# Optimization experiments

Measured on AMD Instinct MI355X. Metric: run time of the kernel, lower is better.

The kernel has to match this reference:

```python
import jax, jax.numpy as jnp
import numpy as np

N_NODES = 163842
N_EDGES = 983040
NUM_FEATURES = 22
LAYER_SIZES = [22, 32, 64, 64]
K = 3  # kernel_size
D = 2  # pseudo-coordinate dim
EPS = 1e-15


def _glorot(key, shape):
    fan = shape[0] + shape[-1]
    s = jnp.sqrt(6.0 / fan)
    return jax.random.uniform(key, shape, jnp.float32, -s, s)


def setup_inputs() -> dict:
    key = jax.random.key(0)
    ks = iter(jax.random.split(key, 64))
    inp = {
        'x': jax.random.normal(next(ks), (N_NODES, NUM_FEATURES), jnp.float32),
        'edge_index': jax.random.randint(next(ks), (2, N_EDGES), 0, N_NODES, jnp.int64),
        'edge_attr': jax.random.uniform(next(ks), (N_EDGES, D), jnp.float32),
    }
    for i, (cin, cout) in enumerate(zip(LAYER_SIZES[:-1], LAYER_SIZES[1:])):
        inp[f'g{i}'] = _glorot(next(ks), (cin, K * cout))
        inp[f'mu{i}'] = _glorot(next(ks), (K, D))
        inp[f'sigma{i}'] = jax.random.uniform(next(ks), (K, D), jnp.float32, 0.5, 1.5)
        inp[f'root{i}'] = _glorot(next(ks), (cin, cout))
        inp[f'b{i}'] = jnp.zeros((cout,), jnp.float32)
    inp['fc_w'] = _glorot(next(ks), (LAYER_SIZES[-1], 2))
    inp['fc_b'] = jnp.zeros((2,), jnp.float32)
    return inp


def gmm_conv(x, src, dst, pseudo, g, mu, sigma, root, bias):
    # PyG GMMConv, separate_gaussians=False, aggr='mean', root_weight=True
    n = x.shape[0]
    cout = root.shape[1]
    xw = (x @ g).reshape(n, K, cout)                       # [N, K, Cout]
    diff = pseudo[:, None, :] - mu[None, :, :]             # [E, K, D]
    gauss = jnp.exp(-0.5 * jnp.sum(diff * diff / (EPS + sigma[None] ** 2), axis=-1))  # [E, K]
    msg = jnp.einsum('ek,eko->eo', gauss, xw[src])         # [E, Cout]
    agg = jax.ops.segment_sum(msg, dst, num_segments=n)
    deg = jax.ops.segment_sum(jnp.ones((src.shape[0],), x.dtype), dst, num_segments=n)
    agg = agg / jnp.clip(deg, 1.0)[:, None]                # mean aggregation
    return agg + x @ root + bias


def reference(x, edge_index, edge_attr, g0, mu0, sigma0, root0, b0,
              g1, mu1, sigma1, root1, b1, g2, mu2, sigma2, root2, b2,
              fc_w, fc_b):
    src, dst = edge_index[0], edge_index[1]
    params = [(g0, mu0, sigma0, root0, b0),
              (g1, mu1, sigma1, root1, b1),
              (g2, mu2, sigma2, root2, b2)]
    h = x
    for (g, mu, sigma, root, b) in params:
        h = jax.nn.relu(gmm_conv(h, src, dst, edge_attr, g, mu, sigma, root, b))
    logits = h @ fc_w + fc_b                               # [N, 2]
    return jax.nn.log_softmax(logits, axis=1)
```

## Files before the change

kernel.cpp:

```cpp
#include <hip/hip_runtime.h>

#define NN 163842
#define NE 983040
#define NB 641
#define BC 32

using short8   = __attribute__((ext_vector_type(8))) short;
using ushort8v = __attribute__((ext_vector_type(8))) unsigned short;
using f32x4    = __attribute__((ext_vector_type(4))) float;

__global__ __launch_bounds__(256) void scatter_bucket(const int* __restrict__ dst,
                                                      int* __restrict__ cnt,
                                                      int* __restrict__ eidx, int E) {
    int e0 = blockIdx.x * 512 + threadIdx.x;
    int e1 = e0 + 256;
    int d0 = (e0 < E) ? dst[e0] : 0;
    int d1 = (e1 < E) ? dst[e1] : 0;
    int p0 = 0, p1 = 0;
    if (e0 < E) p0 = atomicAdd(&cnt[d0], 1);
    if (e1 < E) p1 = atomicAdd(&cnt[d1], 1);
    if (e0 < E && p0 < BC) eidx[d0 * BC + p0] = e0;
    if (e1 < E && p1 < BC) eidx[d1 * BC + p1] = e1;
}

__global__ __launch_bounds__(256) void scan1(const int* __restrict__ degi,
                                             int* __restrict__ cursor,
                                             int* __restrict__ bsum, int n) {
    __shared__ int tmp[256];
    int t = threadIdx.x;
    int i = blockIdx.x * 256 + t;
    int v = (i < n) ? min(degi[i], BC) : 0;
    tmp[t] = v;
    __syncthreads();
    for (int o = 1; o < 256; o <<= 1) {
        int x = (t >= o) ? tmp[t - o] : 0;
        __syncthreads();
        tmp[t] += x;
        __syncthreads();
    }
    if (i < n) cursor[i] = tmp[t] - v;
    if (t == 255) bsum[blockIdx.x] = tmp[255];
}

__global__ void scan2(int* __restrict__ bsum, int nb) {
    __shared__ int tmp[1024];
    int t = threadIdx.x;
    int v = (t < nb) ? bsum[t] : 0;
    tmp[t] = v;
    __syncthreads();
    for (int o = 1; o < 1024; o <<= 1) {
        int x = (t >= o) ? tmp[t - o] : 0;
        __syncthreads();
        tmp[t] += x;
        __syncthreads();
    }
    if (t < nb) bsum[t] = tmp[t] - v;
}

__global__ __launch_bounds__(256) void scan3(int* __restrict__ cursor,
                                             const int* __restrict__ bsum, int n) {
    int i = blockIdx.x * 256 + threadIdx.x;
    if (i < n) cursor[i] += bsum[blockIdx.x];
}

static __device__ __forceinline__ unsigned short bf16rne(float x) {
    unsigned u = __float_as_uint(x);
    u += 0x7FFFu + ((u >> 16) & 1u);
    return (unsigned short)(u >> 16);
}

static __device__ __forceinline__ float bf2f(unsigned short u) {
    return __uint_as_float(((unsigned)u) << 16);
}

template <int CIN, int CINP, int COUTR>
static __device__ __forceinline__ void wcb_emit(int t, const float* __restrict__ g,
                                                const float* __restrict__ root,
                                                unsigned short* __restrict__ Wcb) {
    constexpr int KTl = 4 * CINP;
    int nIdx = t / KTl, k = t - nIdx * KTl;
    int seg = k / CINP, c = k - seg * CINP;
    float v = 0.0f;
    if (c < CIN)
        v = (seg < 3) ? g[c * (3 * COUTR) + seg * COUTR + nIdx] : root[c * COUTR + nIdx];
    Wcb[t] = bf16rne(v);
}

__global__ __launch_bounds__(256) void gather_build(const int* __restrict__ eidx,
                                                    const int* __restrict__ cnt,
                                                    const int* __restrict__ cursor,
                                                    const int* __restrict__ src,
                                                    const float* __restrict__ ea,
                                                    float4* __restrict__ gedr,
                                                    const float* __restrict__ x,
                                                    unsigned short* __restrict__ xp,
                                                    const float* __restrict__ g0, const float* __restrict__ rt0,
                                                    const float* __restrict__ g1, const float* __restrict__ rt1,
                                                    const float* __restrict__ g2, const float* __restrict__ rt2,
                                                    unsigned short* __restrict__ W0,
                                                    unsigned short* __restrict__ W1,
                                                    unsigned short* __restrict__ W2,
                                                    int CBLK, int PBLK, int n) {
    int bid = blockIdx.x;
    if (bid < CBLK) {
        int node = bid * 32 + (threadIdx.x >> 3);
        int li   = threadIdx.x & 7;
        if (node >= n) return;
        int dgc = min(cnt[node], BC);
        int st  = cursor[node];
        for (int c = li; c < dgc; c += 8) {
            int e = eidx[node * BC + c];
            float2 exy = *(const float2*)(ea + 2 * (size_t)e);
            gedr[st + c] = make_float4(__int_as_float(src[e]), exy.x, exy.y, 0.0f);
        }
        return;
    }
    bid -= CBLK;
    if (bid < PBLK) {
        int r = bid * 256 + threadIdx.x;
        if (r >= n) return;
        float v[22];
        const float2* x2 = (const float2*)(x + (size_t)r * 22);
#pragma unroll
        for (int j = 0; j < 11; ++j) *(float2*)(v + 2 * j) = x2[j];
        unsigned short* op = xp + (size_t)r * 32;
#pragma unroll
        for (int g8 = 0; g8 < 4; ++g8) {
            ushort8v o;
#pragma unroll
            for (int j = 0; j < 8; ++j) {
                int c = g8 * 8 + j;
                o[j] = (c < 22) ? bf16rne(v[c]) : (unsigned short)0;
            }
            *(ushort8v*)(op + g8 * 8) = o;
        }
        return;
    }
    bid -= PBLK;
    int t = bid * 256 + threadIdx.x;
    constexpr int T0 = 32 * 128, T1 = 64 * 128, T2 = 64 * 256;
    if (t < T0)                wcb_emit<22, 32, 32>(t, g0, rt0, W0);
    else if (t < T0 + T1)      wcb_emit<32, 32, 64>(t - T0, g1, rt1, W1);
    else if (t < T0 + T1 + T2) wcb_emit<64, 64, 64>(t - T0 - T1, g2, rt2, W2);
}

static __device__ __forceinline__ void fma4(float4& a, float g, const float4& hv) {
    a.x = fmaf(g, hv.x, a.x);
    a.y = fmaf(g, hv.y, a.y);
    a.z = fmaf(g, hv.z, a.z);
    a.w = fmaf(g, hv.w, a.w);
}

static __device__ __forceinline__ float3 gauss3c(float ex, float ey,
                                                 const float* muv, const float* ccv) {
    float3 r;
    float dx, dy;
    dx = ex - muv[0]; dy = ey - muv[1];
    r.x = __expf(fmaf(ccv[0] * dx, dx, ccv[1] * dy * dy));
    dx = ex - muv[2]; dy = ey - muv[3];
    r.y = __expf(fmaf(ccv[2] * dx, dx, ccv[3] * dy * dy));
    dx = ex - muv[4]; dy = ey - muv[5];
    r.z = __expf(fmaf(ccv[4] * dx, dx, ccv[5] * dy * dy));
    return r;
}

template <int CINP, int COUTR, int NT, bool FC>
__global__ __launch_bounds__(NT, 8) void fused_mfma(const unsigned short* __restrict__ h, int hs,
                                                    const float4* __restrict__ ged,
                                                    const int* __restrict__ cursor,
                                                    const int* __restrict__ degi,
                                                    const unsigned short* __restrict__ Wcb,
                                                    const float* __restrict__ bias,
                                                    const float* __restrict__ mu,
                                                    const float* __restrict__ sg,
                                                    unsigned short* __restrict__ out,
                                                    const float* __restrict__ fcw,
                                                    const float* __restrict__ fcb,
                                                    float* __restrict__ fout, int n) {
    constexpr int KT    = 4 * CINP;
    constexpr int ST4   = KT / 8 + 1;
    constexpr int ROWU  = ST4 * 8;
    constexpr int NSTEP = KT / 32;
    constexpr int NCT   = COUTR / 16;
    constexpr int LPN   = CINP / 8;
    constexpr int NPP   = NT / LPN;
    static_assert(NPP == 64, "single pass over the 64-node tile");
    __shared__ float4 sa[64 * ST4];
    unsigned short* st = (unsigned short*)sa;
    const int row0 = blockIdx.x * 64;

    {
        float muv[6], ccv[6];
#pragma unroll
        for (int j = 0; j < 6; ++j) muv[j] = mu[j];
#pragma unroll
        for (int j = 0; j < 6; ++j) {
            float s = sg[j];
            ccv[j] = -0.5f / (1e-15f + s * s);
        }
        const int sub = threadIdx.x / LPN;
        const int li  = threadIdx.x % LPN;
        int node = row0 + sub; if (node > n - 1) node = n - 1;
        int p   = cursor[node];
        int dg  = min(degi[node], BC);
        int end = p + dg;
        float4 a[3][2];
#pragma unroll
        for (int k = 0; k < 3; ++k)
#pragma unroll
            for (int q = 0; q < 2; ++q) a[k][q] = make_float4(0, 0, 0, 0);
        for (; p < end; p += 2) {
            int q1 = (p + 1 < end) ? (p + 1) : p;
            float4 ed0 = ged[p];
            float4 ed1 = ged[q1];
            ushort8v hu0 = *(const ushort8v*)(h + (long)__float_as_int(ed0.x) * hs + li * 8);
            ushort8v hu1 = *(const ushort8v*)(h + (long)__float_as_int(ed1.x) * hs + li * 8);
            float3 g0 = gauss3c(ed0.y, ed0.z, muv, ccv);
            float3 g1 = gauss3c(ed1.y, ed1.z, muv, ccv);
            if (p + 1 >= end) { g1.x = 0.0f; g1.y = 0.0f; g1.z = 0.0f; }
            {
                float4 h0 = make_float4(bf2f(hu0[0]), bf2f(hu0[1]), bf2f(hu0[2]), bf2f(hu0[3]));
                float4 h1 = make_float4(bf2f(hu0[4]), bf2f(hu0[5]), bf2f(hu0[6]), bf2f(hu0[7]));
                fma4(a[0][0], g0.x, h0); fma4(a[0][1], g0.x, h1);
                fma4(a[1][0], g0.y, h0); fma4(a[1][1], g0.y, h1);
                fma4(a[2][0], g0.z, h0); fma4(a[2][1], g0.z, h1);
            }
            {
                float4 h0 = make_float4(bf2f(hu1[0]), bf2f(hu1[1]), bf2f(hu1[2]), bf2f(hu1[3]));
                float4 h1 = make_float4(bf2f(hu1[4]), bf2f(hu1[5]), bf2f(hu1[6]), bf2f(hu1[7]));
                fma4(a[0][0], g1.x, h0); fma4(a[0][1], g1.x, h1);
                fma4(a[1][0], g1.y, h0); fma4(a[1][1], g1.y, h1);
                fma4(a[2][0], g1.z, h0); fma4(a[2][1], g1.z, h1);
            }
        }
        float inv = 1.0f / (float)max(dg, 1);
#pragma unroll
        for (int k = 0; k < 3; ++k)
#pragma unroll
            for (int q = 0; q < 2; ++q) fma4(a[k][q], inv - 1.0f, a[k][q]);
        ushort8v hv8 = *(const ushort8v*)(h + (long)node * hs + li * 8);
        int base = sub * ROWU;
        int c8b  = li * 8;
#pragma unroll
        for (int k = 0; k < 3; ++k) {
            ushort8v v;
            v[0] = bf16rne(a[k][0].x); v[1] = bf16rne(a[k][0].y);
            v[2] = bf16rne(a[k][0].z); v[3] = bf16rne(a[k][0].w);
            v[4] = bf16rne(a[k][1].x); v[5] = bf16rne(a[k][1].y);
            v[6] = bf16rne(a[k][1].z); v[7] = bf16rne(a[k][1].w);
            *(ushort8v*)(st + base + k * CINP + c8b) = v;
        }
        *(ushort8v*)(st + base + 3 * CINP + c8b) = hv8;
    }
    __syncthreads();

    constexpr int NW    = NT / 64;
    constexpr int TILES = 4 * NCT;
    constexpr int TPW   = TILES / NW;
    constexpr int RST   = NW / NCT;
    static_assert(NW % NCT == 0 && TILES % NW == 0, "tile remap");
    const int lane = threadIdx.x & 63;
    const int wv   = threadIdx.x >> 6;
    const int quad = lane >> 4;
    const int c16  = lane & 15;
    const int ct   = wv % NCT;
    const int rg0  = wv / NCT;
    f32x4 acc[TPW];
#pragma unroll
    for (int i = 0; i < TPW; ++i) acc[i] = (f32x4){0.0f, 0.0f, 0.0f, 0.0f};
    const unsigned short* bcol = Wcb + (ct * 16 + c16) * KT;
#pragma unroll
    for (int s = 0; s < NSTEP; ++s) {
        short8 bf = *(const short8*)(bcol + s * 32 + quad * 8);
#pragma unroll
        for (int i = 0; i < TPW; ++i) {
            const unsigned short* arow = st + (16 * (rg0 + i * RST) + c16) * ROWU;
            short8 af = *(const short8*)(arow + s * 32 + quad * 8);
            acc[i] = __builtin_amdgcn_mfma_f32_16x16x32_bf16(af, bf, acc[i], 0, 0, 0);
        }
    }
    if constexpr (!FC) {
#pragma unroll
        for (int i = 0; i < TPW; ++i) {
            int rg  = rg0 + i * RST;
            int col = ct * 16 + c16;
            float b = bias[col];
#pragma unroll
            for (int r = 0; r < 4; ++r) {
                int grow = row0 + rg * 16 + quad * 4 + r;
                if (grow < n)
                    out[(long)grow * COUTR + col] = bf16rne(fmaxf(acc[i][r] + b, 0.0f));
            }
        }
    } else {
        static_assert(COUTR == 64, "FC fusion assumes 64-wide rows");
        constexpr int FS = 72;
        __syncthreads();
        {
            int col = ct * 16 + c16;
            float b = bias[col];
#pragma unroll
            for (int i = 0; i < TPW; ++i) {
                int rg = rg0 + i * RST;
#pragma unroll
                for (int r = 0; r < 4; ++r) {
                    int lr2 = rg * 16 + quad * 4 + r;
                    st[lr2 * FS + col] = bf16rne(fmaxf(acc[i][r] + b, 0.0f));
                }
            }
        }
        __syncthreads();
        int t = threadIdx.x;
        if (t < 64) {
            int node = row0 + t;
            if (node < n) {
                const ushort8v* hr = (const ushort8v*)(st + t * FS);
                float l0 = fcb[0];
                float l1 = fcb[1];
#pragma unroll
                for (int j8 = 0; j8 < 8; ++j8) {
                    ushort8v hv = hr[j8];
#pragma unroll
                    for (int j = 0; j < 8; ++j) {
                        float hvf = bf2f(hv[j]);
                        l0 = fmaf(hvf, fcw[2 * (8 * j8 + j)], l0);
                        l1 = fmaf(hvf, fcw[2 * (8 * j8 + j) + 1], l1);
                    }
                }
                float mx  = fmaxf(l0, l1);
                float lse = mx + logf(__expf(l0 - mx) + __expf(l1 - mx));
                fout[2 * (long)node]     = l0 - lse;
                fout[2 * (long)node + 1] = l1 - lse;
            }
        }
    }
}

extern "C" void kernel_launch(void* const* d_in, const int* in_sizes, int n_in,
                              void* d_out, int out_size, void* d_ws, size_t ws_size,
                              hipStream_t stream) {
    const float* x   = (const float*)d_in[0];
    const int*   ei  = (const int*)d_in[1];
    const float* ea  = (const float*)d_in[2];
    const float* g_[3]  = {(const float*)d_in[3],  (const float*)d_in[8],  (const float*)d_in[13]};
    const float* mu_[3] = {(const float*)d_in[4],  (const float*)d_in[9],  (const float*)d_in[14]};
    const float* sg_[3] = {(const float*)d_in[5],  (const float*)d_in[10], (const float*)d_in[15]};
    const float* rt_[3] = {(const float*)d_in[6],  (const float*)d_in[11], (const float*)d_in[16]};
    const float* bs_[3] = {(const float*)d_in[7],  (const float*)d_in[12], (const float*)d_in[17]};
    const float* fcw = (const float*)d_in[18];
    const float* fcb = (const float*)d_in[19];
    float* out = (float*)d_out;
    (void)in_sizes; (void)n_in; (void)out_size; (void)ws_size;

    char* w = (char*)d_ws;
    size_t off = 0;
    auto carve = [&](size_t bytes) -> void* {
        void* p = (void*)(w + off);
        off += (bytes + 255) & ~(size_t)255;
        return p;
    };
    int*    cnt    = (int*)carve((size_t)NN * 4);
    int*    cursor = (int*)carve((size_t)NN * 4);
    int*    eidx   = (int*)carve((size_t)NN * BC * 4);
    float4* gedr   = (float4*)carve((size_t)NE * 16);
    int*    bsum   = (int*)carve(1024 * 4);
    unsigned short* W0 = (unsigned short*)carve((size_t)32 * 128 * 2);
    unsigned short* W1 = (unsigned short*)carve((size_t)64 * 128 * 2);
    unsigned short* W2 = (unsigned short*)carve((size_t)64 * 256 * 2);
    unsigned short* xp = (unsigned short*)carve((size_t)NN * 32 * 2);
    unsigned short* hA = (unsigned short*)carve((size_t)NN * 32 * 2);
    unsigned short* hB = (unsigned short*)carve((size_t)NN * 64 * 2);

    const int* src = ei;
    const int* dst = ei + NE;
    const int CB = (NN + 31) / 32;
    const int PB = (NN + 255) / 256;
    const int WB = 112;
    const int GB = (NN + 63) / 64;

    hipMemsetAsync(cnt, 0, (size_t)NN * 4, stream);
    scatter_bucket<<<(NE + 511) / 512, 256, 0, stream>>>(dst, cnt, eidx, NE);
    scan1<<<NB, 256, 0, stream>>>(cnt, cursor, bsum, NN);
    scan2<<<1, 1024, 0, stream>>>(bsum, NB);
    scan3<<<NB, 256, 0, stream>>>(cursor, bsum, NN);
    gather_build<<<CB + PB + WB, 256, 0, stream>>>(eidx, cnt, cursor, src, ea, gedr, x, xp,
                                                   g_[0], rt_[0], g_[1], rt_[1], g_[2], rt_[2],
                                                   W0, W1, W2, CB, PB, NN);

    fused_mfma<32, 32, 256, false><<<GB, 256, 0, stream>>>(xp, 32, gedr, cursor, cnt,
                                                           W0, bs_[0], mu_[0], sg_[0],
                                                           hA, nullptr, nullptr,
                                                           nullptr, NN);
    fused_mfma<32, 64, 256, false><<<GB, 256, 0, stream>>>(hA, 32, gedr, cursor, cnt,
                                                           W1, bs_[1], mu_[1], sg_[1],
                                                           hB, nullptr, nullptr,
                                                           nullptr, NN);
    fused_mfma<64, 64, 512, true><<<GB, 512, 0, stream>>>(hB, 64, gedr, cursor, cnt,
                                                          W2, bs_[2], mu_[2], sg_[2],
                                                          nullptr, fcw, fcb,
                                                          out, NN);
}
```

Before: 322.4 us.

## Precompute per-layer Gaussian edge weights in gather pass and use packed float math

The gather pass now evaluates the three Gaussian kernel weights for every edge and every layer once, storing a separate src+weights float4 stream per layer. The fused layer kernels no longer compute exp per edge per lane group. The aggregation loop switches to packed v2f bf16 unpacking and multiply-adds. The workspace is reorganised so the edge bucket array aliases the hidden-state buffers, which avoids a larger allocation. The cost is two extra edge streams written per run, about 32 MB of added write traffic in the preprocessing kernel.

```diff
diff --git a/kernel.cpp b/kernel.cpp
--- a/kernel.cpp
+++ b/kernel.cpp
@@ -8,6 +8,7 @@
 using short8   = __attribute__((ext_vector_type(8))) short;
 using ushort8v = __attribute__((ext_vector_type(8))) unsigned short;
 using f32x4    = __attribute__((ext_vector_type(4))) float;
+using v2f      = __attribute__((ext_vector_type(2))) float;
 
 __global__ __launch_bounds__(256) void scatter_bucket(const int* __restrict__ dst,
                                                       int* __restrict__ cnt,
@@ -69,8 +70,11 @@
     return (unsigned short)(u >> 16);
 }
 
-static __device__ __forceinline__ float bf2f(unsigned short u) {
-    return __uint_as_float(((unsigned)u) << 16);
+static __device__ __forceinline__ v2f bfpair(unsigned u) {
+    v2f r;
+    r[0] = __uint_as_float(u << 16);
+    r[1] = __uint_as_float(u & 0xffff0000u);
+    return r;
 }
 
 template <int CIN, int CINP, int COUTR>
@@ -86,12 +90,30 @@
     Wcb[t] = bf16rne(v);
 }
 
+static __device__ __forceinline__ float3 gauss3c(float ex, float ey,
+                                                 const float* muv, const float* ccv) {
+    float3 r;
+    float dx, dy;
+    dx = ex - muv[0]; dy = ey - muv[1];
+    r.x = __expf(fmaf(ccv[0] * dx, dx, ccv[1] * dy * dy));
+    dx = ex - muv[2]; dy = ey - muv[3];
+    r.y = __expf(fmaf(ccv[2] * dx, dx, ccv[3] * dy * dy));
+    dx = ex - muv[4]; dy = ey - muv[5];
+    r.z = __expf(fmaf(ccv[4] * dx, dx, ccv[5] * dy * dy));
+    return r;
+}
+
 __global__ __launch_bounds__(256) void gather_build(const int* __restrict__ eidx,
                                                     const int* __restrict__ cnt,
                                                     const int* __restrict__ cursor,
                                                     const int* __restrict__ src,
                                                     const float* __restrict__ ea,
-                                                    float4* __restrict__ gedr,
+                                                    const float* __restrict__ mu0, const float* __restrict__ sg0,
+                                                    const float* __restrict__ mu1, const float* __restrict__ sg1,
+                                                    const float* __restrict__ mu2, const float* __restrict__ sg2,
+                                                    float4* __restrict__ ged0,
+                                                    float4* __restrict__ ged1,
+                                                    float4* __restrict__ ged2,
                                                     const float* __restrict__ x,
                                                     unsigned short* __restrict__ xp,
                                                     const float* __restrict__ g0, const float* __restrict__ rt0,
@@ -103,6 +125,15 @@
                                                     int CBLK, int PBLK, int n) {
     int bid = blockIdx.x;
     if (bid < CBLK) {
+        float muv0[6], ccv0[6], muv1[6], ccv1[6], muv2[6], ccv2[6];
+#pragma unroll
+        for (int j = 0; j < 6; ++j) {
+            muv0[j] = mu0[j]; muv1[j] = mu1[j]; muv2[j] = mu2[j];
+            float s0 = sg0[j], s1 = sg1[j], s2 = sg2[j];
+            ccv0[j] = -0.5f / (1e-15f + s0 * s0);
+            ccv1[j] = -0.5f / (1e-15f + s1 * s1);
+            ccv2[j] = -0.5f / (1e-15f + s2 * s2);
+        }
         int node = bid * 32 + (threadIdx.x >> 3);
         int li   = threadIdx.x & 7;
         if (node >= n) return;
@@ -111,7 +142,13 @@
         for (int c = li; c < dgc; c += 8) {
             int e = eidx[node * BC + c];
             float2 exy = *(const float2*)(ea + 2 * (size_t)e);
-            gedr[st + c] = make_float4(__int_as_float(src[e]), exy.x, exy.y, 0.0f);
+            float sb = __int_as_float(src[e]);
+            float3 G0 = gauss3c(exy.x, exy.y, muv0, ccv0);
+            float3 G1 = gauss3c(exy.x, exy.y, muv1, ccv1);
+            float3 G2 = gauss3c(exy.x, exy.y, muv2, ccv2);
+            ged0[st + c] = make_float4(sb, G0.x, G0.y, G0.z);
+            ged1[st + c] = make_float4(sb, G1.x, G1.y, G1.z);
+            ged2[st + c] = make_float4(sb, G2.x, G2.y, G2.z);
         }
         return;
     }
@@ -142,26 +179,6 @@
     if (t < T0)                wcb_emit<22, 32, 32>(t, g0, rt0, W0);
     else if (t < T0 + T1)      wcb_emit<32, 32, 64>(t - T0, g1, rt1, W1);
     else if (t < T0 + T1 + T2) wcb_emit<64, 64, 64>(t - T0 - T1, g2, rt2, W2);
-}
-
-static __device__ __forceinline__ void fma4(float4& a, float g, const float4& hv) {
-    a.x = fmaf(g, hv.x, a.x);
-    a.y = fmaf(g, hv.y, a.y);
-    a.z = fmaf(g, hv.z, a.z);
-    a.w = fmaf(g, hv.w, a.w);
-}
-
-static __device__ __forceinline__ float3 gauss3c(float ex, float ey,
-                                                 const float* muv, const float* ccv) {
-    float3 r;
-    float dx, dy;
-    dx = ex - muv[0]; dy = ey - muv[1];
-    r.x = __expf(fmaf(ccv[0] * dx, dx, ccv[1] * dy * dy));
-    dx = ex - muv[2]; dy = ey - muv[3];
-    r.y = __expf(fmaf(ccv[2] * dx, dx, ccv[3] * dy * dy));
-    dx = ex - muv[4]; dy = ey - muv[5];
-    r.z = __expf(fmaf(ccv[4] * dx, dx, ccv[5] * dy * dy));
-    return r;
 }
 
 template <int CINP, int COUTR, int NT, bool FC>
@@ -171,8 +188,6 @@
                                                     const int* __restrict__ degi,
                                                     const unsigned short* __restrict__ Wcb,
                                                     const float* __restrict__ bias,
-                                                    const float* __restrict__ mu,
-                                                    const float* __restrict__ sg,
                                                     unsigned short* __restrict__ out,
                                                     const float* __restrict__ fcw,
                                                     const float* __restrict__ fcb,
@@ -190,67 +205,62 @@
     const int row0 = blockIdx.x * 64;
 
     {
-        float muv[6], ccv[6];
-#pragma unroll
-        for (int j = 0; j < 6; ++j) muv[j] = mu[j];
-#pragma unroll
-        for (int j = 0; j < 6; ++j) {
-            float s = sg[j];
-            ccv[j] = -0.5f / (1e-15f + s * s);
-        }
         const int sub = threadIdx.x / LPN;
         const int li  = threadIdx.x % LPN;
         int node = row0 + sub; if (node > n - 1) node = n - 1;
         int p   = cursor[node];
         int dg  = min(degi[node], BC);
         int end = p + dg;
-        float4 a[3][2];
+        v2f a[3][4];
 #pragma unroll
         for (int k = 0; k < 3; ++k)
 #pragma unroll
-            for (int q = 0; q < 2; ++q) a[k][q] = make_float4(0, 0, 0, 0);
+            for (int q = 0; q < 4; ++q) a[k][q] = (v2f){0.0f, 0.0f};
         for (; p < end; p += 2) {
             int q1 = (p + 1 < end) ? (p + 1) : p;
             float4 ed0 = ged[p];
             float4 ed1 = ged[q1];
-            ushort8v hu0 = *(const ushort8v*)(h + (long)__float_as_int(ed0.x) * hs + li * 8);
-            ushort8v hu1 = *(const ushort8v*)(h + (long)__float_as_int(ed1.x) * hs + li * 8);
-            float3 g0 = gauss3c(ed0.y, ed0.z, muv, ccv);
-            float3 g1 = gauss3c(ed1.y, ed1.z, muv, ccv);
-            if (p + 1 >= end) { g1.x = 0.0f; g1.y = 0.0f; g1.z = 0.0f; }
+            uint4 hu0 = *(const uint4*)(h + (long)__float_as_int(ed0.x) * hs + li * 8);
+            uint4 hu1 = *(const uint4*)(h + (long)__float_as_int(ed1.x) * hs + li * 8);
+            if (p + 1 >= end) { ed1.y = 0.0f; ed1.z = 0.0f; ed1.w = 0.0f; }
             {
-                float4 h0 = make_float4(bf2f(hu0[0]), bf2f(hu0[1]), bf2f(hu0[2]), bf2f(hu0[3]));
-                float4 h1 = make_float4(bf2f(hu0[4]), bf2f(hu0[5]), bf2f(hu0[6]), bf2f(hu0[7]));
-                fma4(a[0][0], g0.x, h0); fma4(a[0][1], g0.x, h1);
-                fma4(a[1][0], g0.y, h0); fma4(a[1][1], g0.y, h1);
-                fma4(a[2][0], g0.z, h0); fma4(a[2][1], g0.z, h1);
+                v2f hv[4] = {bfpair(hu0.x), bfpair(hu0.y), bfpair(hu0.z), bfpair(hu0.w)};
+#pragma unroll
+                for (int q = 0; q < 4; ++q) {
+                    a[0][q] += hv[q] * ed0.y;
+                    a[1][q] += hv[q] * ed0.z;
+                    a[2][q] += hv[q] * ed0.w;
+                }
             }
             {
-                float4 h0 = make_float4(bf2f(hu1[0]), bf2f(hu1[1]), bf2f(hu1[2]), bf2f(hu1[3]));
-                float4 h1 = make_float4(bf2f(hu1[4]), bf2f(hu1[5]), bf2f(hu1[6]), bf2f(hu1[7]));
-                fma4(a[0][0], g1.x, h0); fma4(a[0][1], g1.x, h1);
-                fma4(a[1][0], g1.y, h0); fma4(a[1][1], g1.y, h1);
-                fma4(a[2][0], g1.z, h0); fma4(a[2][1], g1.z, h1);
+                v2f hv[4] = {bfpair(hu1.x), bfpair(hu1.y), bfpair(hu1.z), bfpair(hu1.w)};
+#pragma unroll
+                for (int q = 0; q < 4; ++q) {
+                    a[0][q] += hv[q] * ed1.y;
+                    a[1][q] += hv[q] * ed1.z;
+                    a[2][q] += hv[q] * ed1.w;
+                }
             }
         }
         float inv = 1.0f / (float)max(dg, 1);
 #pragma unroll
         for (int k = 0; k < 3; ++k)
 #pragma unroll
-            for (int q = 0; q < 2; ++q) fma4(a[k][q], inv - 1.0f, a[k][q]);
-        ushort8v hv8 = *(const ushort8v*)(h + (long)node * hs + li * 8);
+            for (int q = 0; q < 4; ++q) a[k][q] *= inv;
+        uint4 hv4 = *(const uint4*)(h + (long)node * hs + li * 8);
         int base = sub * ROWU;
         int c8b  = li * 8;
 #pragma unroll
         for (int k = 0; k < 3; ++k) {
             ushort8v v;
-            v[0] = bf16rne(a[k][0].x); v[1] = bf16rne(a[k][0].y);
-            v[2] = bf16rne(a[k][0].z); v[3] = bf16rne(a[k][0].w);
-            v[4] = bf16rne(a[k][1].x); v[5] = bf16rne(a[k][1].y);
-            v[6] = bf16rne(a[k][1].z); v[7] = bf16rne(a[k][1].w);
+#pragma unroll
+            for (int q = 0; q < 4; ++q) {
+                v[2 * q]     = bf16rne(a[k][q][0]);
+                v[2 * q + 1] = bf16rne(a[k][q][1]);
+            }
             *(ushort8v*)(st + base + k * CINP + c8b) = v;
         }
-        *(ushort8v*)(st + base + 3 * CINP + c8b) = hv8;
+        *(uint4*)(st + base + 3 * CINP + c8b) = hv4;
     }
     __syncthreads();
 
@@ -322,7 +332,7 @@
                     ushort8v hv = hr[j8];
 #pragma unroll
                     for (int j = 0; j < 8; ++j) {
-                        float hvf = bf2f(hv[j]);
+                        float hvf = __uint_as_float(((unsigned)hv[j]) << 16);
                         l0 = fmaf(hvf, fcw[2 * (8 * j8 + j)], l0);
                         l1 = fmaf(hvf, fcw[2 * (8 * j8 + j) + 1], l1);
                     }
@@ -361,15 +371,18 @@
     };
     int*    cnt    = (int*)carve((size_t)NN * 4);
     int*    cursor = (int*)carve((size_t)NN * 4);
-    int*    eidx   = (int*)carve((size_t)NN * BC * 4);
-    float4* gedr   = (float4*)carve((size_t)NE * 16);
     int*    bsum   = (int*)carve(1024 * 4);
+    float4* ged0   = (float4*)carve((size_t)NE * 16);
+    float4* ged1   = (float4*)carve((size_t)NE * 16);
+    float4* ged2   = (float4*)carve((size_t)NE * 16);
     unsigned short* W0 = (unsigned short*)carve((size_t)32 * 128 * 2);
     unsigned short* W1 = (unsigned short*)carve((size_t)64 * 128 * 2);
     unsigned short* W2 = (unsigned short*)carve((size_t)64 * 256 * 2);
     unsigned short* xp = (unsigned short*)carve((size_t)NN * 32 * 2);
-    unsigned short* hA = (unsigned short*)carve((size_t)NN * 32 * 2);
-    unsigned short* hB = (unsigned short*)carve((size_t)NN * 64 * 2);
+    char* uni = (char*)carve((size_t)NN * 64 * 2 + (size_t)NN * 32 * 2);
+    int*            eidx = (int*)uni;
+    unsigned short* hA   = (unsigned short*)uni;
+    unsigned short* hB   = (unsigned short*)(uni + (size_t)NN * 32 * 2);
 
     const int* src = ei;
     const int* dst = ei + NE;
@@ -383,20 +396,19 @@
     scan1<<<NB, 256, 0, stream>>>(cnt, cursor, bsum, NN);
     scan2<<<1, 1024, 0, stream>>>(bsum, NB);
     scan3<<<NB, 256, 0, stream>>>(cursor, bsum, NN);
-    gather_build<<<CB + PB + WB, 256, 0, stream>>>(eidx, cnt, cursor, src, ea, gedr, x, xp,
+    gather_build<<<CB + PB + WB, 256, 0, stream>>>(eidx, cnt, cursor, src, ea,
+                                                   mu_[0], sg_[0], mu_[1], sg_[1], mu_[2], sg_[2],
+                                                   ged0, ged1, ged2, x, xp,
                                                    g_[0], rt_[0], g_[1], rt_[1], g_[2], rt_[2],
                                                    W0, W1, W2, CB, PB, NN);
 
-    fused_mfma<32, 32, 256, false><<<GB, 256, 0, stream>>>(xp, 32, gedr, cursor, cnt,
-                                                           W0, bs_[0], mu_[0], sg_[0],
-                                                           hA, nullptr, nullptr,
+    fused_mfma<32, 32, 256, false><<<GB, 256, 0, stream>>>(xp, 32, ged0, cursor, cnt,
+                                                           W0, bs_[0], hA, nullptr, nullptr,
                                                            nullptr, NN);
-    fused_mfma<32, 64, 256, false><<<GB, 256, 0, stream>>>(hA, 32, gedr, cursor, cnt,
-                                                           W1, bs_[1], mu_[1], sg_[1],
-                                                           hB, nullptr, nullptr,
+    fused_mfma<32, 64, 256, false><<<GB, 256, 0, stream>>>(hA, 32, ged1, cursor, cnt,
+                                                           W1, bs_[1], hB, nullptr, nullptr,
                                                            nullptr, NN);
-    fused_mfma<64, 64, 512, true><<<GB, 512, 0, stream>>>(hB, 64, gedr, cursor, cnt,
-                                                          W2, bs_[2], mu_[2], sg_[2],
-                                                          nullptr, fcw, fcb,
+    fused_mfma<64, 64, 512, true><<<GB, 512, 0, stream>>>(hB, 64, ged2, cursor, cnt,
+                                                          W2, bs_[2], nullptr, fcw, fcb,
                                                           out, NN);
 }
```

New measurement: 324.0 us. Within noise of the previous version (+0.5%).
